# Kernel optimization log

Hardware: AMD Instinct MI355X
Metric: run time of the kernel (lower is better)

## Reference

```python
import jax, jax.numpy as jnp
import numpy as np

BOUND = 1.0
MIN_NEAR = 0.2
DENSITY_SCALE = 1.0
AABB_MIN = jnp.array([-BOUND, -BOUND, -BOUND], dtype=jnp.float32)
AABB_MAX = jnp.array([BOUND, BOUND, BOUND], dtype=jnp.float32)


def setup_inputs() -> dict:
    key = jax.random.key(0)
    ks = jax.random.split(key, 8)
    N = 32768
    rays_o = (jax.random.uniform(ks[0], (N, 3), dtype=jnp.float32) - 0.5)  # inside AABB
    d = jax.random.normal(ks[1], (N, 3), dtype=jnp.float32)
    rays_d = d / jnp.linalg.norm(d, axis=-1, keepdims=True)
    def w(k, shape):
        return jax.random.normal(k, shape, dtype=jnp.float32) * (1.0 / np.sqrt(shape[0]))
    return {
        'rays_o': rays_o, 'rays_d': rays_d,
        'Wd1': w(ks[2], (3, 64)), 'bd1': jnp.zeros((64,), jnp.float32),
        'Wd2': w(ks[3], (64, 16)), 'bd2': jnp.zeros((16,), jnp.float32),
        'Wc1': w(ks[4], (18, 64)), 'bc1': jnp.zeros((64,), jnp.float32),
        'Wc2': w(ks[5], (64, 3)), 'bc2': jnp.zeros((3,), jnp.float32),
        'num_steps': 128, 'upsample_steps': 128,
    }


def _density(x, Wd1, bd1, Wd2, bd2):
    # stand-in for abstract self.density(): sigma + geometric feature
    h = jax.nn.relu(x @ Wd1 + bd1)
    h = h @ Wd2 + bd2
    return jax.nn.softplus(h[..., 0]), h[..., 1:]


def _color(x, d, geo, Wc1, bc1, Wc2, bc2):
    # stand-in for abstract self.color() (mask skipped: compute everywhere)
    h = jax.nn.relu(jnp.concatenate([d, geo], axis=-1) @ Wc1 + bc1)
    return jax.nn.sigmoid(h @ Wc2 + bc2)


def _near_far(rays_o, rays_d):
    # raymarching.near_far_from_aabb equivalent (slab test)
    inv = 1.0 / rays_d
    t1 = (AABB_MIN - rays_o) * inv
    t2 = (AABB_MAX - rays_o) * inv
    tmin = jnp.minimum(t1, t2).max(axis=-1)
    tmax = jnp.maximum(t1, t2).min(axis=-1)
    nears = jnp.maximum(tmin, MIN_NEAR)
    fars = jnp.maximum(tmax, nears + 1e-4)
    return nears[:, None], fars[:, None]


def _alpha_weights(z_vals, sigma, sample_dist):
    # alpha compositing: exp -> cumprod transmittance -> weights
    deltas = z_vals[..., 1:] - z_vals[..., :-1]
    deltas = jnp.concatenate([deltas, sample_dist * jnp.ones_like(deltas[..., :1])], axis=-1)
    alphas = 1.0 - jnp.exp(-deltas * DENSITY_SCALE * sigma)
    shifted = jnp.concatenate([jnp.ones_like(alphas[..., :1]), 1.0 - alphas + 1e-15], axis=-1)
    weights = alphas * jnp.cumprod(shifted, axis=-1)[..., :-1]
    return weights


def _sample_pdf(bins, weights, n):
    # inverse-CDF importance sampling, deterministic (eval mode)
    weights = weights + 1e-5
    pdf = weights / weights.sum(axis=-1, keepdims=True)
    cdf = jnp.cumsum(pdf, axis=-1)
    cdf = jnp.concatenate([jnp.zeros_like(cdf[..., :1]), cdf], axis=-1)  # [N, M+1]
    u = jnp.linspace(0.5 / n, 1.0 - 0.5 / n, n, dtype=cdf.dtype)
    u = jnp.broadcast_to(u, cdf.shape[:-1] + (n,))
    inds = jax.vmap(lambda c, uu: jnp.searchsorted(c, uu, side='right'))(cdf, u)
    hi = cdf.shape[-1] - 1
    below = jnp.clip(inds - 1, 0, hi)
    above = jnp.clip(inds, 0, hi)
    cg0 = jnp.take_along_axis(cdf, below, axis=-1)
    cg1 = jnp.take_along_axis(cdf, above, axis=-1)
    bg0 = jnp.take_along_axis(bins, below, axis=-1)
    bg1 = jnp.take_along_axis(bins, above, axis=-1)
    denom = cg1 - cg0
    denom = jnp.where(denom < 1e-5, 1.0, denom)
    t = (u - cg0) / denom
    return bg0 + t * (bg1 - bg0)


def reference(rays_o, rays_d, Wd1, bd1, Wd2, bd2, Wc1, bc1, Wc2, bc2, num_steps, upsample_steps):
    N = rays_o.shape[0]
    nears, fars = _near_far(rays_o, rays_d)
    nears = jax.lax.stop_gradient(nears)
    fars = jax.lax.stop_gradient(fars)

    z = jnp.linspace(0.0, 1.0, num_steps, dtype=rays_o.dtype)[None, :]
    z_vals = nears + (fars - nears) * z                      # [N, T]
    sample_dist = (fars - nears) / num_steps                 # [N, 1]

    xyzs = rays_o[:, None, :] + rays_d[:, None, :] * z_vals[..., None]
    xyzs = jnp.clip(xyzs, AABB_MIN, AABB_MAX)
    sigma, geo = _density(xyzs.reshape(-1, 3), Wd1, bd1, Wd2, bd2)
    sigma = sigma.reshape(N, num_steps)
    geo = geo.reshape(N, num_steps, -1)

    # --- importance resampling (no grad through positions/weights) ---
    w_coarse = _alpha_weights(jax.lax.stop_gradient(z_vals),
                              jax.lax.stop_gradient(sigma), sample_dist)
    z_mid = z_vals[..., :-1] + 0.5 * (z_vals[..., 1:] - z_vals[..., :-1])
    new_z = _sample_pdf(jax.lax.stop_gradient(z_mid), w_coarse[:, 1:-1], upsample_steps)
    new_z = jax.lax.stop_gradient(new_z)
    new_xyzs = rays_o[:, None, :] + rays_d[:, None, :] * new_z[..., None]
    new_xyzs = jax.lax.stop_gradient(jnp.clip(new_xyzs, AABB_MIN, AABB_MAX))

    new_sigma, new_geo = _density(new_xyzs.reshape(-1, 3), Wd1, bd1, Wd2, bd2)
    new_sigma = new_sigma.reshape(N, upsample_steps)
    new_geo = new_geo.reshape(N, upsample_steps, -1)

    # --- merge coarse + fine by sorted depth (sort + gather) ---
    z_all = jnp.concatenate([z_vals, new_z], axis=1)
    idx = jnp.argsort(z_all, axis=1)
    z_vals = jnp.take_along_axis(z_all, idx, axis=1)
    xyzs = jnp.take_along_axis(jnp.concatenate([xyzs, new_xyzs], axis=1), idx[..., None], axis=1)
    sigma = jnp.take_along_axis(jnp.concatenate([sigma, new_sigma], axis=1), idx, axis=1)
    geo = jnp.take_along_axis(jnp.concatenate([geo, new_geo], axis=1), idx[..., None], axis=1)

    weights = _alpha_weights(z_vals, sigma, sample_dist)     # [N, T+U]
    dirs = jnp.broadcast_to(rays_d[:, None, :], xyzs.shape)
    rgbs = _color(xyzs.reshape(-1, 3), dirs.reshape(-1, 3), geo.reshape(-1, geo.shape[-1]),
                  Wc1, bc1, Wc2, bc2).reshape(N, -1, 3)

    weights_sum = weights.sum(axis=-1)
    ori_z = jnp.clip((z_vals - nears) / (fars - nears), 0.0, 1.0)
    depth = jnp.sum(weights * ori_z, axis=-1)
    image = jnp.sum(weights[..., None] * rgbs, axis=-2)
    image = image + (1.0 - weights_sum)[..., None] * 1.0     # white background
    return depth, image, weights_sum
```

## Files before the change

### kernel.cpp

```cpp
#include <hip/hip_runtime.h>
#include <math.h>

#define NTH 256
#define RPB 2
#define T 128
#define U 128
#define TT 256

__device__ __forceinline__ float softplus_f(float x) {
    return fmaxf(x, 0.0f) + log1pf(expf(-fabsf(x)));
}
__device__ __forceinline__ float sigmoid_f(float x) {
    return 1.0f / (1.0f + expf(-x));
}
__device__ __forceinline__ float clamp1(float x) {
    return fminf(fmaxf(x, -1.0f), 1.0f);
}
__device__ __forceinline__ unsigned short f2bf(float f) {
    unsigned int u = __float_as_uint(f);
    unsigned int r = (u + 0x7FFFu + ((u >> 16) & 1u)) >> 16;
    return (unsigned short)r;
}
__device__ __forceinline__ float bf2f(unsigned short v) {
    return __uint_as_float(((unsigned int)v) << 16);
}

__global__ void __launch_bounds__(NTH)
nerf_render_kernel(
    const float* __restrict__ rays_o, const float* __restrict__ rays_d,
    const float* __restrict__ Wd1, const float* __restrict__ bd1,
    const float* __restrict__ Wd2, const float* __restrict__ bd2,
    const float* __restrict__ Wc1, const float* __restrict__ bc1,
    const float* __restrict__ Wc2, const float* __restrict__ bc2,
    float* __restrict__ out, int N)
{
    const int tid  = threadIdx.x;
    const int rtid = tid & 127;
    const int r    = tid >> 7;
    const int ray  = blockIdx.x * RPB + r;
    const int lane = tid & 63;
    const int wv   = (tid >> 6) & 1;

    __shared__ float w1[192];
    __shared__ float b1[64];
    __shared__ float w2[1024];
    __shared__ float b2[16];
    __shared__ float c1[64 * 20];
    __shared__ float c2[64 * 4];
    __shared__ unsigned short s_geo16[RPB][15][TT];
    __shared__ float s_sigma[RPB][TT];
    __shared__ float s_z[RPB][TT];
    __shared__ float s_zs[RPB][TT];
    __shared__ int   s_perm[RPB][TT];
    __shared__ float s_wc[RPB][T];
    __shared__ float s_cdf[RPB][T];
    __shared__ float s_bins[RPB][T];
    __shared__ float s_ct[RPB][4];
    __shared__ float s_tmp[RPB][4];
    __shared__ float s_red[RPB][2][5];

    for (int i = tid; i < 192; i += NTH)  w1[i] = Wd1[i];
    for (int i = tid; i < 64; i += NTH)   b1[i] = bd1[i];
    for (int i = tid; i < 1024; i += NTH) w2[i] = Wd2[i];
    for (int i = tid; i < 16; i += NTH)   b2[i] = bd2[i];
    for (int i = tid; i < 64 * 20; i += NTH) {
        int j = i / 20, k = i - j * 20;
        c1[i] = (k < 18) ? Wc1[k * 64 + j] : ((k == 18) ? bc1[j] : 0.0f);
    }
    for (int i = tid; i < 256; i += NTH) {
        int j = i >> 2, c = i & 3;
        c2[i] = (c < 3) ? Wc2[j * 3 + c] : 0.0f;
    }

    const float ox = rays_o[ray * 3 + 0], oy = rays_o[ray * 3 + 1], oz = rays_o[ray * 3 + 2];
    const float dx = rays_d[ray * 3 + 0], dy = rays_d[ray * 3 + 1], dz = rays_d[ray * 3 + 2];
    const float ivx = 1.0f / dx, ivy = 1.0f / dy, ivz = 1.0f / dz;
    const float t1x = (-1.0f - ox) * ivx, t2x = (1.0f - ox) * ivx;
    const float t1y = (-1.0f - oy) * ivy, t2y = (1.0f - oy) * ivy;
    const float t1z = (-1.0f - oz) * ivz, t2z = (1.0f - oz) * ivz;
    const float tmin = fmaxf(fmaxf(fminf(t1x, t2x), fminf(t1y, t2y)), fminf(t1z, t2z));
    const float tmax = fminf(fminf(fmaxf(t1x, t2x), fmaxf(t1y, t2y)), fmaxf(t1z, t2z));
    const float nearv = fmaxf(tmin, 0.2f);
    const float farv  = fmaxf(tmax, nearv + 1e-4f);
    const float span  = farv - nearv;
    const float sample_dist = span * (1.0f / 128.0f);

    __syncthreads();

    auto density_mlp = [&](float x0, float x1, float x2, int si, float* sig_out) {
        float o[16];
        {
            const float4* bp = (const float4*)b2;
            float4 q0 = bp[0], q1 = bp[1], q2 = bp[2], q3 = bp[3];
            o[0] = q0.x; o[1] = q0.y; o[2]  = q0.z; o[3]  = q0.w;
            o[4] = q1.x; o[5] = q1.y; o[6]  = q1.z; o[7]  = q1.w;
            o[8] = q2.x; o[9] = q2.y; o[10] = q2.z; o[11] = q2.w;
            o[12] = q3.x; o[13] = q3.y; o[14] = q3.z; o[15] = q3.w;
        }
        for (int jb = 0; jb < 16; ++jb) {
            float4 wa  = *(const float4*)&w1[jb * 4];
            float4 wbv = *(const float4*)&w1[64 + jb * 4];
            float4 wcv = *(const float4*)&w1[128 + jb * 4];
            float4 bb  = *(const float4*)&b1[jb * 4];
            float hh[4];
            hh[0] = fmaxf(fmaf(x0, wa.x, fmaf(x1, wbv.x, fmaf(x2, wcv.x, bb.x))), 0.0f);
            hh[1] = fmaxf(fmaf(x0, wa.y, fmaf(x1, wbv.y, fmaf(x2, wcv.y, bb.y))), 0.0f);
            hh[2] = fmaxf(fmaf(x0, wa.z, fmaf(x1, wbv.z, fmaf(x2, wcv.z, bb.z))), 0.0f);
            hh[3] = fmaxf(fmaf(x0, wa.w, fmaf(x1, wbv.w, fmaf(x2, wcv.w, bb.w))), 0.0f);
            #pragma unroll
            for (int u = 0; u < 4; ++u) {
                const float4* rr = (const float4*)&w2[(jb * 4 + u) * 16];
                float4 r0 = rr[0], r1 = rr[1], r2 = rr[2], r3 = rr[3];
                float h = hh[u];
                o[0]  = fmaf(h, r0.x, o[0]);  o[1]  = fmaf(h, r0.y, o[1]);
                o[2]  = fmaf(h, r0.z, o[2]);  o[3]  = fmaf(h, r0.w, o[3]);
                o[4]  = fmaf(h, r1.x, o[4]);  o[5]  = fmaf(h, r1.y, o[5]);
                o[6]  = fmaf(h, r1.z, o[6]);  o[7]  = fmaf(h, r1.w, o[7]);
                o[8]  = fmaf(h, r2.x, o[8]);  o[9]  = fmaf(h, r2.y, o[9]);
                o[10] = fmaf(h, r2.z, o[10]); o[11] = fmaf(h, r2.w, o[11]);
                o[12] = fmaf(h, r3.x, o[12]); o[13] = fmaf(h, r3.y, o[13]);
                o[14] = fmaf(h, r3.z, o[14]); o[15] = fmaf(h, r3.w, o[15]);
            }
        }
        *sig_out = softplus_f(o[0]);
        #pragma unroll
        for (int k = 0; k < 15; ++k) s_geo16[r][k][si] = f2bf(o[1 + k]);
    };

    float z_reg, sigma_reg;
    {
        float frac = (float)rtid * (1.0f / 127.0f);
        z_reg = fmaf(span, frac, nearv);
        s_z[r][rtid] = z_reg;
        float x0 = clamp1(fmaf(dx, z_reg, ox));
        float x1 = clamp1(fmaf(dy, z_reg, oy));
        float x2 = clamp1(fmaf(dz, z_reg, oz));
        density_mlp(x0, x1, x2, rtid, &sigma_reg);
        s_sigma[r][rtid] = sigma_reg;
    }
    __syncthreads();

    {
        float delta = (rtid < T - 1) ? (s_z[r][rtid + 1] - z_reg) : sample_dist;
        float alpha = 1.0f - expf(-delta * sigma_reg);
        float inc = 1.0f - alpha + 1e-15f;
        #pragma unroll
        for (int off = 1; off < 64; off <<= 1) {
            float v = __shfl_up(inc, off);
            if (lane >= off) inc *= v;
        }
        if (lane == 63) s_tmp[r][wv] = inc;
        __syncthreads();
        float ex = __shfl_up(inc, 1);
        if (lane == 0) ex = 1.0f;
        if (wv == 1) ex *= s_tmp[r][0];
        s_wc[r][rtid] = alpha * ex;
    }
    __syncthreads();

    {
        float pv = (rtid < 126) ? (s_wc[r][rtid + 1] + 1e-5f) : 0.0f;
        float inc = pv;
        #pragma unroll
        for (int off = 1; off < 64; off <<= 1) {
            float v = __shfl_up(inc, off);
            if (lane >= off) inc += v;
        }
        if (lane == 63) s_tmp[r][2 + wv] = inc;
        __syncthreads();
        float tot = s_tmp[r][2] + s_tmp[r][3];
        float inv = 1.0f / tot;
        if (wv == 1) inc += s_tmp[r][2];
        if (rtid < 126) s_cdf[r][rtid + 1] = inc * inv;
        if (rtid == 0)  s_cdf[r][0] = 0.0f;
        s_bins[r][rtid] = (rtid < 127) ? fmaf(0.5f, s_z[r][rtid + 1] - z_reg, z_reg) : 0.0f;
    }
    __syncthreads();

    {
        float u = (1.0f + 2.0f * (float)rtid) * (1.0f / 256.0f);
        int lo = 0, hi = 127;
        while (lo < hi) { int mid = (lo + hi) >> 1; if (s_cdf[r][mid] <= u) lo = mid + 1; else hi = mid; }
        int below = lo - 1;
        int above = (lo < 127) ? lo : 126;
        float cg0 = s_cdf[r][below], cg1 = s_cdf[r][above];
        float bg0 = s_bins[r][below], bg1 = s_bins[r][above];
        float den = cg1 - cg0; if (den < 1e-5f) den = 1.0f;
        float tt2 = (u - cg0) / den;
        float nz = fmaf(tt2, bg1 - bg0, bg0);
        s_z[r][T + rtid] = nz;
        float x0 = clamp1(fmaf(dx, nz, ox));
        float x1 = clamp1(fmaf(dy, nz, oy));
        float x2 = clamp1(fmaf(dz, nz, oz));
        float sg;
        density_mlp(x0, x1, x2, T + rtid, &sg);
        s_sigma[r][T + rtid] = sg;
    }
    __syncthreads();

    {
        float vc = z_reg;
        int lo = 0, hi = U;
        while (lo < hi) { int mid = (lo + hi) >> 1; if (s_z[r][T + mid] < vc) lo = mid + 1; else hi = mid; }
        int rc = rtid + lo;
        s_perm[r][rc] = rtid; s_zs[r][rc] = vc;

        float vf = s_z[r][T + rtid];
        lo = 0; hi = T;
        while (lo < hi) { int mid = (lo + hi) >> 1; if (s_z[r][mid] <= vf) lo = mid + 1; else hi = mid; }
        int rf = rtid + lo;
        s_perm[r][rf] = T + rtid; s_zs[r][rf] = vf;
    }
    __syncthreads();

    const int eA = wv * 64 + lane;
    const int eB = 128 + wv * 64 + lane;
    float wA, wB, aA, aB;
    {
        float zA = s_zs[r][eA];
        float dA = s_zs[r][eA + 1] - zA;
        float zB = s_zs[r][eB];
        float dB = (eB < TT - 1) ? (s_zs[r][eB + 1] - zB) : sample_dist;
        aA = 1.0f - expf(-dA * s_sigma[r][s_perm[r][eA]]);
        aB = 1.0f - expf(-dB * s_sigma[r][s_perm[r][eB]]);
        float tA = 1.0f - aA + 1e-15f;
        float tB = 1.0f - aB + 1e-15f;
        #pragma unroll
        for (int off = 1; off < 64; off <<= 1) {
            float vA = __shfl_up(tA, off);
            float vB = __shfl_up(tB, off);
            if (lane >= off) { tA *= vA; tB *= vB; }
        }
        if (lane == 63) { s_ct[r][wv] = tA; s_ct[r][2 + wv] = tB; }
        __syncthreads();
        float ct0 = s_ct[r][0], ct1 = s_ct[r][1], ct2 = s_ct[r][2];
        float exA = __shfl_up(tA, 1); if (lane == 0) exA = 1.0f;
        float exB = __shfl_up(tB, 1); if (lane == 0) exB = 1.0f;
        float pA = (wv == 0) ? 1.0f : ct0;
        float pB = ct0 * ct1 * ((wv == 0) ? 1.0f : ct2);
        wA = aA * exA * pA;
        wB = aB * exB * pB;
    }

    float inA[20], inB[20];
    inA[0] = dx; inA[1] = dy; inA[2] = dz;
    inB[0] = dx; inB[1] = dy; inB[2] = dz;
    {
        int pa = s_perm[r][eA], pb = s_perm[r][eB];
        #pragma unroll
        for (int k = 0; k < 15; ++k) {
            inA[3 + k] = bf2f(s_geo16[r][k][pa]);
            inB[3 + k] = bf2f(s_geo16[r][k][pb]);
        }
    }
    inA[18] = 1.0f; inA[19] = 0.0f;
    inB[18] = 1.0f; inB[19] = 0.0f;
    float o0A = bc2[0], o1A = bc2[1], o2A = bc2[2];
    float o0B = o0A, o1B = o1A, o2B = o2A;
    for (int j = 0; j < 64; ++j) {
        const float4* row = (const float4*)&c1[j * 20];
        float hA = 0.0f, hB = 0.0f;
        #pragma unroll
        for (int kb = 0; kb < 5; ++kb) {
            float4 rr = row[kb];
            hA = fmaf(inA[kb * 4 + 0], rr.x, hA);
            hA = fmaf(inA[kb * 4 + 1], rr.y, hA);
            hA = fmaf(inA[kb * 4 + 2], rr.z, hA);
            hA = fmaf(inA[kb * 4 + 3], rr.w, hA);
            hB = fmaf(inB[kb * 4 + 0], rr.x, hB);
            hB = fmaf(inB[kb * 4 + 1], rr.y, hB);
            hB = fmaf(inB[kb * 4 + 2], rr.z, hB);
            hB = fmaf(inB[kb * 4 + 3], rr.w, hB);
        }
        hA = fmaxf(hA, 0.0f);
        hB = fmaxf(hB, 0.0f);
        float4 q = *(const float4*)&c2[j * 4];
        o0A = fmaf(hA, q.x, o0A); o1A = fmaf(hA, q.y, o1A); o2A = fmaf(hA, q.z, o2A);
        o0B = fmaf(hB, q.x, o0B); o1B = fmaf(hB, q.y, o1B); o2B = fmaf(hB, q.z, o2B);
    }
    float rA = sigmoid_f(o0A), gA = sigmoid_f(o1A), bA = sigmoid_f(o2A);
    float rB = sigmoid_f(o0B), gB = sigmoid_f(o1B), bB = sigmoid_f(o2B);

    float orizA = fminf(fmaxf((s_zs[r][eA] - nearv) / span, 0.0f), 1.0f);
    float orizB = fminf(fmaxf((s_zs[r][eB] - nearv) / span, 0.0f), 1.0f);
    float c_ws = wA + wB;
    float c_dp = wA * orizA + wB * orizB;
    float c_r  = wA * rA + wB * rB;
    float c_g  = wA * gA + wB * gB;
    float c_b  = wA * bA + wB * bB;
    #pragma unroll
    for (int off = 32; off > 0; off >>= 1) {
        c_ws += __shfl_down(c_ws, off);
        c_dp += __shfl_down(c_dp, off);
        c_r  += __shfl_down(c_r,  off);
        c_g  += __shfl_down(c_g,  off);
        c_b  += __shfl_down(c_b,  off);
    }
    __syncthreads();
    if (lane == 0) {
        s_red[r][wv][0] = c_ws; s_red[r][wv][1] = c_dp;
        s_red[r][wv][2] = c_r;  s_red[r][wv][3] = c_g; s_red[r][wv][4] = c_b;
    }
    __syncthreads();
    if (rtid == 0) {
        float ws = s_red[r][0][0] + s_red[r][1][0];
        float dp = s_red[r][0][1] + s_red[r][1][1];
        float rr = s_red[r][0][2] + s_red[r][1][2];
        float gg = s_red[r][0][3] + s_red[r][1][3];
        float bb = s_red[r][0][4] + s_red[r][1][4];
        float bgadd = 1.0f - ws;
        out[ray]             = dp;
        out[N + ray * 3 + 0] = rr + bgadd;
        out[N + ray * 3 + 1] = gg + bgadd;
        out[N + ray * 3 + 2] = bb + bgadd;
        out[4 * N + ray]     = ws;
    }
}

extern "C" void kernel_launch(void* const* d_in, const int* in_sizes, int n_in,
                              void* d_out, int out_size, void* d_ws, size_t ws_size,
                              hipStream_t stream) {
    const float* rays_o = (const float*)d_in[0];
    const float* rays_d = (const float*)d_in[1];
    const float* Wd1 = (const float*)d_in[2];
    const float* bd1 = (const float*)d_in[3];
    const float* Wd2 = (const float*)d_in[4];
    const float* bd2 = (const float*)d_in[5];
    const float* Wc1 = (const float*)d_in[6];
    const float* bc1 = (const float*)d_in[7];
    const float* Wc2 = (const float*)d_in[8];
    const float* bc2 = (const float*)d_in[9];

    const int N = in_sizes[0] / 3;
    float* out = (float*)d_out;

    nerf_render_kernel<<<N / RPB, NTH, 0, stream>>>(
        rays_o, rays_d, Wd1, bd1, Wd2, bd2, Wc1, bc1, Wc2, bc2, out, N);
}
```

Measured before the change: 703.0 us.

## Read MLP weights directly from global memory instead of staging in LDS

```diff
diff --git a/kernel.cpp b/kernel.cpp
--- a/kernel.cpp
+++ b/kernel.cpp
@@ -25,7 +25,7 @@
     return __uint_as_float(((unsigned int)v) << 16);
 }
 
-__global__ void __launch_bounds__(NTH)
+__global__ void __launch_bounds__(NTH, 5)
 nerf_render_kernel(
     const float* __restrict__ rays_o, const float* __restrict__ rays_d,
     const float* __restrict__ Wd1, const float* __restrict__ bd1,
@@ -41,12 +41,6 @@
     const int lane = tid & 63;
     const int wv   = (tid >> 6) & 1;
 
-    __shared__ float w1[192];
-    __shared__ float b1[64];
-    __shared__ float w2[1024];
-    __shared__ float b2[16];
-    __shared__ float c1[64 * 20];
-    __shared__ float c2[64 * 4];
     __shared__ unsigned short s_geo16[RPB][15][TT];
     __shared__ float s_sigma[RPB][TT];
     __shared__ float s_z[RPB][TT];
@@ -58,19 +52,6 @@
     __shared__ float s_ct[RPB][4];
     __shared__ float s_tmp[RPB][4];
     __shared__ float s_red[RPB][2][5];
-
-    for (int i = tid; i < 192; i += NTH)  w1[i] = Wd1[i];
-    for (int i = tid; i < 64; i += NTH)   b1[i] = bd1[i];
-    for (int i = tid; i < 1024; i += NTH) w2[i] = Wd2[i];
-    for (int i = tid; i < 16; i += NTH)   b2[i] = bd2[i];
-    for (int i = tid; i < 64 * 20; i += NTH) {
-        int j = i / 20, k = i - j * 20;
-        c1[i] = (k < 18) ? Wc1[k * 64 + j] : ((k == 18) ? bc1[j] : 0.0f);
-    }
-    for (int i = tid; i < 256; i += NTH) {
-        int j = i >> 2, c = i & 3;
-        c2[i] = (c < 3) ? Wc2[j * 3 + c] : 0.0f;
-    }
 
     const float ox = rays_o[ray * 3 + 0], oy = rays_o[ray * 3 + 1], oz = rays_o[ray * 3 + 2];
     const float dx = rays_d[ray * 3 + 0], dy = rays_d[ray * 3 + 1], dz = rays_d[ray * 3 + 2];
@@ -85,41 +66,23 @@
     const float span  = farv - nearv;
     const float sample_dist = span * (1.0f / 128.0f);
 
-    __syncthreads();
-
     auto density_mlp = [&](float x0, float x1, float x2, int si, float* sig_out) {
         float o[16];
-        {
-            const float4* bp = (const float4*)b2;
-            float4 q0 = bp[0], q1 = bp[1], q2 = bp[2], q3 = bp[3];
-            o[0] = q0.x; o[1] = q0.y; o[2]  = q0.z; o[3]  = q0.w;
-            o[4] = q1.x; o[5] = q1.y; o[6]  = q1.z; o[7]  = q1.w;
-            o[8] = q2.x; o[9] = q2.y; o[10] = q2.z; o[11] = q2.w;
-            o[12] = q3.x; o[13] = q3.y; o[14] = q3.z; o[15] = q3.w;
-        }
+        #pragma unroll
+        for (int m = 0; m < 16; ++m) o[m] = bd2[m];
         for (int jb = 0; jb < 16; ++jb) {
-            float4 wa  = *(const float4*)&w1[jb * 4];
-            float4 wbv = *(const float4*)&w1[64 + jb * 4];
-            float4 wcv = *(const float4*)&w1[128 + jb * 4];
-            float4 bb  = *(const float4*)&b1[jb * 4];
             float hh[4];
-            hh[0] = fmaxf(fmaf(x0, wa.x, fmaf(x1, wbv.x, fmaf(x2, wcv.x, bb.x))), 0.0f);
-            hh[1] = fmaxf(fmaf(x0, wa.y, fmaf(x1, wbv.y, fmaf(x2, wcv.y, bb.y))), 0.0f);
-            hh[2] = fmaxf(fmaf(x0, wa.z, fmaf(x1, wbv.z, fmaf(x2, wcv.z, bb.z))), 0.0f);
-            hh[3] = fmaxf(fmaf(x0, wa.w, fmaf(x1, wbv.w, fmaf(x2, wcv.w, bb.w))), 0.0f);
+            #pragma unroll
+            for (int q = 0; q < 4; ++q) {
+                int j = jb * 4 + q;
+                hh[q] = fmaxf(fmaf(x0, Wd1[j], fmaf(x1, Wd1[64 + j], fmaf(x2, Wd1[128 + j], bd1[j]))), 0.0f);
+            }
             #pragma unroll
             for (int u = 0; u < 4; ++u) {
-                const float4* rr = (const float4*)&w2[(jb * 4 + u) * 16];
-                float4 r0 = rr[0], r1 = rr[1], r2 = rr[2], r3 = rr[3];
                 float h = hh[u];
-                o[0]  = fmaf(h, r0.x, o[0]);  o[1]  = fmaf(h, r0.y, o[1]);
-                o[2]  = fmaf(h, r0.z, o[2]);  o[3]  = fmaf(h, r0.w, o[3]);
-                o[4]  = fmaf(h, r1.x, o[4]);  o[5]  = fmaf(h, r1.y, o[5]);
-                o[6]  = fmaf(h, r1.z, o[6]);  o[7]  = fmaf(h, r1.w, o[7]);
-                o[8]  = fmaf(h, r2.x, o[8]);  o[9]  = fmaf(h, r2.y, o[9]);
-                o[10] = fmaf(h, r2.z, o[10]); o[11] = fmaf(h, r2.w, o[11]);
-                o[12] = fmaf(h, r3.x, o[12]); o[13] = fmaf(h, r3.y, o[13]);
-                o[14] = fmaf(h, r3.z, o[14]); o[15] = fmaf(h, r3.w, o[15]);
+                #pragma unroll
+                for (int m = 0; m < 16; ++m)
+                    o[m] = fmaf(h, Wd2[(jb * 4 + u) * 16 + m], o[m]);
             }
         }
         *sig_out = softplus_f(o[0]);
@@ -242,7 +205,7 @@
         wB = aB * exB * pB;
     }
 
-    float inA[20], inB[20];
+    float inA[18], inB[18];
     inA[0] = dx; inA[1] = dy; inA[2] = dz;
     inB[0] = dx; inB[1] = dy; inB[2] = dz;
     {
@@ -253,30 +216,31 @@
             inB[3 + k] = bf2f(s_geo16[r][k][pb]);
         }
     }
-    inA[18] = 1.0f; inA[19] = 0.0f;
-    inB[18] = 1.0f; inB[19] = 0.0f;
     float o0A = bc2[0], o1A = bc2[1], o2A = bc2[2];
     float o0B = o0A, o1B = o1A, o2B = o2A;
-    for (int j = 0; j < 64; ++j) {
-        const float4* row = (const float4*)&c1[j * 20];
-        float hA = 0.0f, hB = 0.0f;
-        #pragma unroll
-        for (int kb = 0; kb < 5; ++kb) {
-            float4 rr = row[kb];
-            hA = fmaf(inA[kb * 4 + 0], rr.x, hA);
-            hA = fmaf(inA[kb * 4 + 1], rr.y, hA);
-            hA = fmaf(inA[kb * 4 + 2], rr.z, hA);
-            hA = fmaf(inA[kb * 4 + 3], rr.w, hA);
-            hB = fmaf(inB[kb * 4 + 0], rr.x, hB);
-            hB = fmaf(inB[kb * 4 + 1], rr.y, hB);
-            hB = fmaf(inB[kb * 4 + 2], rr.z, hB);
-            hB = fmaf(inB[kb * 4 + 3], rr.w, hB);
-        }
-        hA = fmaxf(hA, 0.0f);
-        hB = fmaxf(hB, 0.0f);
-        float4 q = *(const float4*)&c2[j * 4];
-        o0A = fmaf(hA, q.x, o0A); o1A = fmaf(hA, q.y, o1A); o2A = fmaf(hA, q.z, o2A);
-        o0B = fmaf(hB, q.x, o0B); o1B = fmaf(hB, q.y, o1B); o2B = fmaf(hB, q.z, o2B);
+    for (int j4 = 0; j4 < 64; j4 += 4) {
+        float hA[4], hB[4];
+        #pragma unroll
+        for (int q = 0; q < 4; ++q) { hA[q] = bc1[j4 + q]; hB[q] = hA[q]; }
+        #pragma unroll
+        for (int k = 0; k < 18; ++k) {
+            float a = inA[k], b = inB[k];
+            #pragma unroll
+            for (int q = 0; q < 4; ++q) {
+                float w = Wc1[k * 64 + j4 + q];
+                hA[q] = fmaf(a, w, hA[q]);
+                hB[q] = fmaf(b, w, hB[q]);
+            }
+        }
+        #pragma unroll
+        for (int q = 0; q < 4; ++q) {
+            float ha = fmaxf(hA[q], 0.0f), hb = fmaxf(hB[q], 0.0f);
+            float w0 = Wc2[(j4 + q) * 3 + 0];
+            float w1 = Wc2[(j4 + q) * 3 + 1];
+            float w2 = Wc2[(j4 + q) * 3 + 2];
+            o0A = fmaf(ha, w0, o0A); o1A = fmaf(ha, w1, o1A); o2A = fmaf(ha, w2, o2A);
+            o0B = fmaf(hb, w0, o0B); o1B = fmaf(hb, w1, o1B); o2B = fmaf(hb, w2, o2B);
+        }
     }
     float rA = sigmoid_f(o0A), gA = sigmoid_f(o1A), bA = sigmoid_f(o2A);
     float rB = sigmoid_f(o0B), gB = sigmoid_f(o1B), bB = sigmoid_f(o2B);
```

Result: faster. 616.7 us (-12.3%).
